# Kernel tuning notes

Measured on AMD Instinct MI355X. Metric: run time of the kernel, lower is better.

Reference implementation:

```python
import jax, jax.numpy as jnp
import numpy as np
from jax import lax


def setup_inputs() -> dict:
    key = jax.random.key(0)
    k1, k2, k3 = jax.random.split(key, 3)
    B, C, H, W = 32, 256, 64, 64
    x = jax.random.normal(k1, (B, C, H, W), dtype=jnp.float32)
    # ECA conv1d: 1 in-ch, 1 out-ch, kernel 5 (derived from C=256), no bias
    conv1d_w = jax.random.normal(k2, (1, 1, 5), dtype=jnp.float32) * 0.3
    # Spatial conv2d: 2 in-ch, 1 out-ch, kernel 7, with bias
    conv2d_w = jax.random.normal(k3, (1, 2, 7, 7), dtype=jnp.float32) * 0.1
    conv2d_b = jnp.zeros((1,), dtype=jnp.float32)
    return {"x": x, "conv1d_w": conv1d_w, "conv2d_w": conv2d_w, "conv2d_b": conv2d_b}


def reference(x, conv1d_w, conv2d_w, conv2d_b):
    # --- ECA channel attention ---
    # global avg pool over H,W -> [B, C]
    y = jnp.mean(x, axis=(2, 3))
    # conv1d across the channel axis (treated as length), 1 feature channel
    y = y[:, None, :]  # [B, 1, C]
    y = lax.conv_general_dilated(
        y, conv1d_w, window_strides=(1,), padding=[(2, 2)],
        dimension_numbers=("NCH", "OIH", "NCH"))
    ch_w = jax.nn.sigmoid(y)[:, 0, :, None, None]  # [B, C, 1, 1]
    eca_out = x * ch_w

    # --- spatial attention ---
    max_pool = jnp.max(x, axis=1, keepdims=True)   # [B,1,H,W]
    avg_pool = jnp.mean(x, axis=1, keepdims=True)  # [B,1,H,W]
    sp_in = jnp.concatenate([max_pool, avg_pool], axis=1)  # [B,2,H,W]
    sp = lax.conv_general_dilated(
        sp_in, conv2d_w, window_strides=(1, 1), padding=[(3, 3), (3, 3)],
        dimension_numbers=("NCHW", "OIHW", "NCHW"))
    sp = jax.nn.sigmoid(sp + conv2d_b[None, :, None, None])  # [B,1,H,W]

    return eca_out + x * sp + x
```

## Files before the change

kernel.cpp:

```cpp
#include <hip/hip_runtime.h>
#include <math.h>

#define BB 32
#define CC 256
#define HH 64
#define WW 64
#define HWSZ (HH * WW)

__device__ inline void atomicMaxFloat(float* addr, float val) {
  if (val >= 0.0f) atomicMax((int*)addr, __float_as_int(val));
  else             atomicMin((unsigned int*)addr, __float_as_uint(val));
}

__global__ __launch_bounds__(256) void stats_kernel(
    const float* __restrict__ x, float* __restrict__ chan_sum,
    float* __restrict__ pool_max, float* __restrict__ pool_sum) {
  const int b = blockIdx.x >> 6;
  const int rem = blockIdx.x & 63;
  const int cchunk = rem >> 2;
  const int hwchunk = rem & 3;
  const int c0 = cchunk << 4;
  const int hw0 = (hwchunk << 10) + (threadIdx.x << 2);

  const float4* xp = (const float4*)(x + ((size_t)b << 20) + ((size_t)c0 << 12) + hw0);

  float4 mx = make_float4(-3.4e38f, -3.4e38f, -3.4e38f, -3.4e38f);
  float4 sm = make_float4(0.f, 0.f, 0.f, 0.f);
  float s[16];

#pragma unroll
  for (int ci = 0; ci < 16; ++ci) {
    const float4 v = xp[ci * (HWSZ / 4)];
    mx.x = fmaxf(mx.x, v.x); mx.y = fmaxf(mx.y, v.y);
    mx.z = fmaxf(mx.z, v.z); mx.w = fmaxf(mx.w, v.w);
    sm.x += v.x; sm.y += v.y; sm.z += v.z; sm.w += v.w;
    s[ci] = (v.x + v.y) + (v.z + v.w);
  }

  const int pidx = (b << 12) + hw0;
  atomicMaxFloat(&pool_max[pidx + 0], mx.x);
  atomicMaxFloat(&pool_max[pidx + 1], mx.y);
  atomicMaxFloat(&pool_max[pidx + 2], mx.z);
  atomicMaxFloat(&pool_max[pidx + 3], mx.w);
  atomicAdd(&pool_sum[pidx + 0], sm.x);
  atomicAdd(&pool_sum[pidx + 1], sm.y);
  atomicAdd(&pool_sum[pidx + 2], sm.z);
  atomicAdd(&pool_sum[pidx + 3], sm.w);

#pragma unroll
  for (int ci = 0; ci < 16; ++ci) {
    float v = s[ci];
#pragma unroll
    for (int off = 32; off > 0; off >>= 1) v += __shfl_xor(v, off, 64);
    if ((threadIdx.x & 63) == 0) atomicAdd(&chan_sum[b * CC + c0 + ci], v);
  }
}

__global__ __launch_bounds__(256) void eca_kernel(
    const float* __restrict__ chan_sum, const float* __restrict__ w5,
    float* __restrict__ ch_w) {
  __shared__ float m[CC];
  const int b = blockIdx.x;
  const int c = threadIdx.x;
  m[c] = chan_sum[b * CC + c] * (1.0f / HWSZ);
  __syncthreads();

  float acc = 0.0f;
#pragma unroll
  for (int k = 0; k < 5; ++k) {
    int cc = c + k - 2;
    float v = (cc >= 0 && cc < CC) ? m[cc] : 0.0f;
    acc = fmaf(v, w5[k], acc);
  }
  ch_w[b * CC + c] = 1.0f / (1.0f + __expf(-acc));
}

__global__ __launch_bounds__(256) void spatial_kernel(
    const float* __restrict__ pool_max, const float* __restrict__ pool_sum,
    const float* __restrict__ w2, const float* __restrict__ bias,
    float* __restrict__ sp) {
  const int idx = blockIdx.x * 256 + threadIdx.x;
  const int b = idx >> 12;
  const int hw = idx & (HWSZ - 1);
  const int h = hw >> 6;
  const int w = hw & 63;

  float acc = bias[0];
#pragma unroll
  for (int kh = 0; kh < 7; ++kh) {
    const int hh = h + kh - 3;
    if (hh < 0 || hh >= HH) continue;
#pragma unroll
    for (int kw = 0; kw < 7; ++kw) {
      const int ww = w + kw - 3;
      if (ww < 0 || ww >= WW) continue;
      const int off = b * HWSZ + hh * WW + ww;
      acc = fmaf(pool_max[off], w2[kh * 7 + kw], acc);
      acc = fmaf(pool_sum[off], w2[49 + kh * 7 + kw] * (1.0f / CC), acc);
    }
  }
  sp[idx] = 1.0f / (1.0f + __expf(-acc));
}

__global__ __launch_bounds__(256) void combine_kernel(
    const float* __restrict__ x, const float* __restrict__ ch_w,
    const float* __restrict__ sp, float* __restrict__ out) {
  const size_t f = (size_t)blockIdx.x * 256 + threadIdx.x;
  const size_t e = f * 4;
  const int b = (int)(e >> 20);
  const int c = (int)(e >> 12) & 255;
  const int hw = (int)e & (HWSZ - 1);

  const float4 x4 = ((const float4*)x)[f];
  const float4 s4 = ((const float4*)(sp + ((size_t)b << 12)))[hw >> 2];
  const float cw = ch_w[b * CC + c] + 1.0f;

  float4 o;
  o.x = x4.x * (cw + s4.x);
  o.y = x4.y * (cw + s4.y);
  o.z = x4.z * (cw + s4.z);
  o.w = x4.w * (cw + s4.w);
  ((float4*)out)[f] = o;
}

extern "C" void kernel_launch(void* const* d_in, const int* in_sizes, int n_in,
                              void* d_out, int out_size, void* d_ws, size_t ws_size,
                              hipStream_t stream) {
  const float* x    = (const float*)d_in[0];
  const float* w1   = (const float*)d_in[1];
  const float* w2   = (const float*)d_in[2];
  const float* bias = (const float*)d_in[3];
  float* out = (float*)d_out;

  float* ws = (float*)d_ws;
  float* chan_sum = ws;
  float* ch_w     = ws + 8192;
  float* pool_sum = ws + 16384;
  float* pool_max = ws + 147456;
  float* sp       = ws + 278528;

  hipMemsetAsync(ws, 0, (size_t)147456 * sizeof(float), stream);
  hipMemsetAsync(pool_max, 0xFF, (size_t)131072 * sizeof(float), stream);

  stats_kernel<<<BB * 64, 256, 0, stream>>>(x, chan_sum, pool_max, pool_sum);
  eca_kernel<<<BB, 256, 0, stream>>>(chan_sum, w1, ch_w);
  spatial_kernel<<<(BB * HWSZ) / 256, 256, 0, stream>>>(pool_max, pool_sum, w2, bias, sp);
  combine_kernel<<<(BB * CC * HWSZ) / (4 * 256), 256, 0, stream>>>(x, ch_w, sp, out);
}
```

Before: 296.6 us.

## Replace atomic reductions in stats kernel with block-local reduction and partial buffers

Stats blocks now span all channels for a 256-position spatial chunk, reducing max/sum across waves in shared memory and storing results directly instead of using global atomics. Channel sums are written as per-chunk partials and summed in the ECA kernel, eliminating the workspace memsets. Fewer, longer-running blocks may reduce memory-level parallelism.

```diff
diff --git a/kernel.cpp b/kernel.cpp
--- a/kernel.cpp
+++ b/kernel.cpp
@@ -6,63 +6,87 @@
 #define HH 64
 #define WW 64
 #define HWSZ (HH * WW)
+#define NCHUNK 16
 
-__device__ inline void atomicMaxFloat(float* addr, float val) {
-  if (val >= 0.0f) atomicMax((int*)addr, __float_as_int(val));
-  else             atomicMin((unsigned int*)addr, __float_as_uint(val));
-}
+__global__ __launch_bounds__(256, 2) void stats_kernel(
+    const float* __restrict__ x, float* __restrict__ chan_part,
+    float* __restrict__ pool_max, float* __restrict__ pool_sum) {
+  const int b = blockIdx.x >> 4;
+  const int chunk = blockIdx.x & 15;
+  const int hw0 = chunk << 8;
+  const int tid = threadIdx.x;
+  const int wave = tid >> 6;
+  const int lane = tid & 63;
+  const int c_base = wave << 6;
 
-__global__ __launch_bounds__(256) void stats_kernel(
-    const float* __restrict__ x, float* __restrict__ chan_sum,
-    float* __restrict__ pool_max, float* __restrict__ pool_sum) {
-  const int b = blockIdx.x >> 6;
-  const int rem = blockIdx.x & 63;
-  const int cchunk = rem >> 2;
-  const int hwchunk = rem & 3;
-  const int c0 = cchunk << 4;
-  const int hw0 = (hwchunk << 10) + (threadIdx.x << 2);
-
-  const float4* xp = (const float4*)(x + ((size_t)b << 20) + ((size_t)c0 << 12) + hw0);
+  const float4* xp =
+      (const float4*)(x + ((size_t)b << 20) + ((size_t)c_base << 12) + hw0) + lane;
 
   float4 mx = make_float4(-3.4e38f, -3.4e38f, -3.4e38f, -3.4e38f);
   float4 sm = make_float4(0.f, 0.f, 0.f, 0.f);
-  float s[16];
 
+  for (int g = 0; g < 4; ++g) {
+    float s[16];
 #pragma unroll
-  for (int ci = 0; ci < 16; ++ci) {
-    const float4 v = xp[ci * (HWSZ / 4)];
-    mx.x = fmaxf(mx.x, v.x); mx.y = fmaxf(mx.y, v.y);
-    mx.z = fmaxf(mx.z, v.z); mx.w = fmaxf(mx.w, v.w);
-    sm.x += v.x; sm.y += v.y; sm.z += v.z; sm.w += v.w;
-    s[ci] = (v.x + v.y) + (v.z + v.w);
+    for (int ci = 0; ci < 16; ++ci) {
+      const float4 v = xp[(g * 16 + ci) * (HWSZ / 4)];
+      mx.x = fmaxf(mx.x, v.x); mx.y = fmaxf(mx.y, v.y);
+      mx.z = fmaxf(mx.z, v.z); mx.w = fmaxf(mx.w, v.w);
+      sm.x += v.x; sm.y += v.y; sm.z += v.z; sm.w += v.w;
+      s[ci] = (v.x + v.y) + (v.z + v.w);
+    }
+#pragma unroll
+    for (int ci = 0; ci < 16; ++ci) {
+      float v = s[ci];
+#pragma unroll
+      for (int off = 32; off > 0; off >>= 1) v += __shfl_xor(v, off, 64);
+      s[ci] = v;
+    }
+    if (lane == 0) {
+      float4* cp = (float4*)(chan_part +
+                             ((size_t)(b * NCHUNK + chunk)) * CC + c_base + g * 16);
+      cp[0] = make_float4(s[0],  s[1],  s[2],  s[3]);
+      cp[1] = make_float4(s[4],  s[5],  s[6],  s[7]);
+      cp[2] = make_float4(s[8],  s[9],  s[10], s[11]);
+      cp[3] = make_float4(s[12], s[13], s[14], s[15]);
+    }
   }
 
-  const int pidx = (b << 12) + hw0;
-  atomicMaxFloat(&pool_max[pidx + 0], mx.x);
-  atomicMaxFloat(&pool_max[pidx + 1], mx.y);
-  atomicMaxFloat(&pool_max[pidx + 2], mx.z);
-  atomicMaxFloat(&pool_max[pidx + 3], mx.w);
-  atomicAdd(&pool_sum[pidx + 0], sm.x);
-  atomicAdd(&pool_sum[pidx + 1], sm.y);
-  atomicAdd(&pool_sum[pidx + 2], sm.z);
-  atomicAdd(&pool_sum[pidx + 3], sm.w);
-
-#pragma unroll
-  for (int ci = 0; ci < 16; ++ci) {
-    float v = s[ci];
-#pragma unroll
-    for (int off = 32; off > 0; off >>= 1) v += __shfl_xor(v, off, 64);
-    if ((threadIdx.x & 63) == 0) atomicAdd(&chan_sum[b * CC + c0 + ci], v);
+  __shared__ float4 lmax[4][64];
+  __shared__ float4 lsum[4][64];
+  lmax[wave][lane] = mx;
+  lsum[wave][lane] = sm;
+  __syncthreads();
+  if (tid < 64) {
+    const float4 a = lmax[0][tid], b4 = lmax[1][tid];
+    const float4 c4 = lmax[2][tid], d4 = lmax[3][tid];
+    float4 M;
+    M.x = fmaxf(fmaxf(a.x, b4.x), fmaxf(c4.x, d4.x));
+    M.y = fmaxf(fmaxf(a.y, b4.y), fmaxf(c4.y, d4.y));
+    M.z = fmaxf(fmaxf(a.z, b4.z), fmaxf(c4.z, d4.z));
+    M.w = fmaxf(fmaxf(a.w, b4.w), fmaxf(c4.w, d4.w));
+    const float4 sa = lsum[0][tid], sb = lsum[1][tid];
+    const float4 sc = lsum[2][tid], sd = lsum[3][tid];
+    float4 S;
+    S.x = (sa.x + sb.x) + (sc.x + sd.x);
+    S.y = (sa.y + sb.y) + (sc.y + sd.y);
+    S.z = (sa.z + sb.z) + (sc.z + sd.z);
+    S.w = (sa.w + sb.w) + (sc.w + sd.w);
+    ((float4*)(pool_max + ((size_t)b << 12) + hw0))[tid] = M;
+    ((float4*)(pool_sum + ((size_t)b << 12) + hw0))[tid] = S;
   }
 }
 
 __global__ __launch_bounds__(256) void eca_kernel(
-    const float* __restrict__ chan_sum, const float* __restrict__ w5,
+    const float* __restrict__ chan_part, const float* __restrict__ w5,
     float* __restrict__ ch_w) {
   __shared__ float m[CC];
   const int b = blockIdx.x;
   const int c = threadIdx.x;
-  m[c] = chan_sum[b * CC + c] * (1.0f / HWSZ);
+  float s = 0.0f;
+#pragma unroll
+  for (int k = 0; k < NCHUNK; ++k) s += chan_part[(size_t)(b * NCHUNK + k) * CC + c];
+  m[c] = s * (1.0f / HWSZ);
   __syncthreads();
 
   float acc = 0.0f;
@@ -133,17 +157,14 @@
   float* out = (float*)d_out;
 
   float* ws = (float*)d_ws;
-  float* chan_sum = ws;
-  float* ch_w     = ws + 8192;
-  float* pool_sum = ws + 16384;
-  float* pool_max = ws + 147456;
-  float* sp       = ws + 278528;
+  float* chan_part = ws;
+  float* ch_w      = ws + 131072;
+  float* pool_max  = ws + 139264;
+  float* pool_sum  = ws + 270336;
+  float* sp        = ws + 401408;
 
-  hipMemsetAsync(ws, 0, (size_t)147456 * sizeof(float), stream);
-  hipMemsetAsync(pool_max, 0xFF, (size_t)131072 * sizeof(float), stream);
-
-  stats_kernel<<<BB * 64, 256, 0, stream>>>(x, chan_sum, pool_max, pool_sum);
-  eca_kernel<<<BB, 256, 0, stream>>>(chan_sum, w1, ch_w);
+  stats_kernel<<<BB * NCHUNK, 256, 0, stream>>>(x, chan_part, pool_max, pool_sum);
+  eca_kernel<<<BB, 256, 0, stream>>>(chan_part, w1, ch_w);
   spatial_kernel<<<(BB * HWSZ) / 256, 256, 0, stream>>>(pool_max, pool_sum, w2, bias, sp);
   combine_kernel<<<(BB * CC * HWSZ) / (4 * 256), 256, 0, stream>>>(x, ch_w, sp, out);
 }
```

Result: faster. 259.3 us (-12.6%).
